# Optimization experiments

Hardware: AMD Instinct MI355X
Metric: run time of the kernel (lower is better)

## Reference

```python
import jax, jax.numpy as jnp
import numpy as np

VAR0, VAR1 = 0.1, 0.2
POS_TH, NEG_TH = 0.5, 0.5
NEG_POS_RATIO = 10

def point_form(c):
    # center-size (cx,cy,w,h) -> corners (x1,y1,x2,y2)
    return jnp.concatenate([c[..., :2] - c[..., 2:] / 2, c[..., :2] + c[..., 2:] / 2], axis=-1)

def iou(a, b):
    # corner-form boxes, broadcastable [..., 4]
    lt = jnp.maximum(a[..., :2], b[..., :2])
    rb = jnp.minimum(a[..., 2:], b[..., 2:])
    wh = jnp.clip(rb - lt, 0.0)
    inter = wh[..., 0] * wh[..., 1]
    area_a = (a[..., 2] - a[..., 0]) * (a[..., 3] - a[..., 1])
    area_b = (b[..., 2] - b[..., 0]) * (b[..., 3] - b[..., 1])
    return inter / (area_a + area_b - inter)

def encode(matched, priors):
    # matched: corner-form gt boxes; priors: center-size anchors
    g_cxcy = ((matched[..., :2] + matched[..., 2:]) * 0.5 - priors[..., :2]) / (VAR0 * priors[..., 2:])
    g_wh = jnp.log((matched[..., 2:] - matched[..., :2]) / priors[..., 2:]) / VAR1
    return jnp.concatenate([g_cxcy, g_wh], axis=-1)

def smooth_l1(d):
    ad = jnp.abs(d)
    return jnp.where(ad < 1.0, 0.5 * ad * ad, ad - 0.5)

def setup_inputs() -> dict:
    key = jax.random.key(0)
    ks = jax.random.split(key, 8)
    B, O, A = 8, 32, 16384
    cxy = jax.random.uniform(ks[0], (A, 2), minval=0.1, maxval=0.9)
    wh = jax.random.uniform(ks[1], (A, 2), minval=0.05, maxval=0.3)
    anchors = jnp.concatenate([cxy, wh], axis=-1)  # [A,4] center-size
    # ground-truth boxes jittered around random anchors so matching finds positives
    idx = jax.random.randint(ks[2], (B, O), 0, A)
    base = point_form(anchors)[idx]  # [B,O,4] corner form
    boxes = base + jax.random.uniform(ks[3], (B, O, 4), minval=-0.01, maxval=0.01)
    counts = jax.random.randint(ks[4], (B,), 4, O)  # valid objects per image
    pad = jnp.arange(O)[None, :] >= counts[:, None]
    cls = jax.random.randint(ks[5], (B, O), 0, 2)
    true_classes = jnp.where(pad, -1, cls).astype(jnp.int32)
    true_boxes = jnp.where(pad[..., None], -1.0, boxes)
    pred_boxes = 0.5 * jax.random.normal(ks[6], (B, A, 4))
    pred_classes = jax.random.normal(ks[7], (B, A, 2))
    return dict(pred_boxes=pred_boxes, pred_classes=pred_classes,
                true_boxes=true_boxes, true_classes=true_classes, anchors=anchors)

def detection_loss(pred_boxes, pred_classes, true_boxes, true_classes, anchors):
    dtype = pred_boxes.dtype
    pad = true_classes < 0  # [B,O]
    # --- anchor matching (IoU between corner-form anchors and gt boxes) ---
    overlap = iou(point_form(anchors)[None, None, :, :], true_boxes[:, :, None, :])  # [B,O,A]
    overlap = jnp.where(pad[..., None], -1.0, overlap)
    best = overlap.max(axis=1, keepdims=True)  # best gt per anchor
    positive = (jnp.abs(best - overlap) < 1e-6) & (overlap > POS_TH)  # [B,O,A]
    negative = overlap.max(axis=1) < NEG_TH  # [B,A]
    n_pos = positive.sum()
    denom = jnp.maximum(n_pos, 1).astype(dtype)
    # --- box loss: SmoothL1(sum) on encoded positives only ---
    dummy = jnp.array([0.3, 0.3, 0.5, 0.5], dtype)  # valid dummy box for padded slots (masked out)
    tb = jnp.where(pad[..., None], dummy, true_boxes)
    enc = encode(tb[:, :, None, :], anchors[None, None, :, :])  # [B,O,A,4]
    d = jnp.where(positive[..., None], pred_boxes[:, None, :, :] - enc, 0.0)
    box_loss = 1.0 * smooth_l1(d).sum() / denom
    # --- class loss: positives + hard-negative mining, weighted CE mean ---
    logp = jax.nn.log_softmax(pred_classes, axis=-1)  # [B,A,2]
    cls = jnp.clip(true_classes, 0, 1)
    ce_pos = -jnp.where((cls == 1)[:, :, None], logp[:, None, :, 1], logp[:, None, :, 0])  # [B,O,A]
    w = jnp.where(cls == 1, 4.0, 1.0)[:, :, None]
    sum_pos = jnp.sum(positive * w * ce_pos)
    wsum_pos = jnp.sum(positive * w)
    # negatives: target class 0 (weight 1); mining rank == CE value
    neg_ce = jnp.where(negative, -logp[..., 0], -jnp.inf).reshape(-1)  # [B*A]
    sorted_desc = jnp.sort(neg_ce)[::-1]
    n_neg = negative.sum()
    k = jnp.minimum(NEG_POS_RATIO * n_pos, n_neg)
    take = jnp.arange(sorted_desc.shape[0]) < k
    sum_neg = jnp.sum(jnp.where(take, sorted_desc, 0.0))
    cls_loss = 10.0 * (sum_pos + sum_neg) / jnp.maximum(wsum_pos + k.astype(dtype), 1e-6) / denom
    total = box_loss + cls_loss
    return box_loss, cls_loss, total

def reference(pred_boxes, pred_classes, true_boxes, true_classes, anchors):
    return detection_loss(pred_boxes, pred_classes, true_boxes, true_classes, anchors)
```

## Files before the change

kernel.cpp:

```cpp
#include <hip/hip_runtime.h>
#include <math.h>

#define NOBJ  32
#define NANCH 16384
#define NTOT  131072
#define MBLK  256
#define NREP  16

#define OFF_SLOTS 64
#define OFF_HC    2112
#define HWORDS    (NREP * 8192)

__device__ __forceinline__ float smooth_l1f(float d) {
    float ad = fabsf(d);
    return ad < 1.0f ? 0.5f * ad * ad : ad - 0.5f;
}

__global__ __launch_bounds__(256) void dl_zero(unsigned int* __restrict__ ws)
{
    int i = blockIdx.x * 256 + threadIdx.x;
    reinterpret_cast<uint4*>(ws + OFF_HC)[i] = make_uint4(0u, 0u, 0u, 0u);
}

__global__ __launch_bounds__(512) void dl_main(
    const float* __restrict__ pred_boxes,
    const float* __restrict__ pred_classes,
    const float* __restrict__ true_boxes,
    const int*   __restrict__ true_classes,
    const float* __restrict__ anchors,
    unsigned int* __restrict__ ws)
{
    __shared__ float    s_tb[NOBJ * 4];
    __shared__ int      s_tc[NOBJ];
    __shared__ unsigned lcnt[4096];
    __shared__ float    lsum[4096];
    __shared__ int      s_wi[8][2];
    __shared__ float    s_wf[8][3];

    const int t = threadIdx.x;
    const int idx = blockIdx.x * 512 + t;
    const int b = idx >> 14;
    const int a = idx & (NANCH - 1);
    if (t < NOBJ * 4) s_tb[t] = true_boxes[b * NOBJ * 4 + t];
    if (t < NOBJ)     s_tc[t] = true_classes[b * NOBJ + t];
    for (int i = t; i < 4096; i += 512) { lcnt[i] = 0u; lsum[i] = 0.f; }
    __syncthreads();

    float4 anc = reinterpret_cast<const float4*>(anchors)[a];
    float ax1 = anc.x - anc.z * 0.5f;
    float ay1 = anc.y - anc.w * 0.5f;
    float ax2 = anc.x + anc.z * 0.5f;
    float ay2 = anc.y + anc.w * 0.5f;
    float area_a = (ax2 - ax1) * (ay2 - ay1);

    float ov[NOBJ];
    float best = -3.402823466e38f;
#pragma unroll
    for (int o = 0; o < NOBJ; ++o) {
        float v;
        if (s_tc[o] < 0) {
            v = -1.0f;
        } else {
            float bx1 = s_tb[o * 4 + 0], by1 = s_tb[o * 4 + 1];
            float bx2 = s_tb[o * 4 + 2], by2 = s_tb[o * 4 + 3];
            float ltx = fmaxf(ax1, bx1), lty = fmaxf(ay1, by1);
            float rbx = fminf(ax2, bx2), rby = fminf(ay2, by2);
            float w = fmaxf(rbx - ltx, 0.0f), h = fmaxf(rby - lty, 0.0f);
            float inter = w * h;
            float area_b = (bx2 - bx1) * (by2 - by1);
            v = inter / (area_a + area_b - inter);
        }
        ov[o] = v;
        best = fmaxf(best, v);
    }

    float2 pc = reinterpret_cast<const float2*>(pred_classes)[idx];
    float mx = fmaxf(pc.x, pc.y);
    float lse = mx + logf(expf(pc.x - mx) + expf(pc.y - mx));
    float l0 = pc.x - lse;
    float l1 = pc.y - lse;

    int isneg = 0;
    if (best < 0.5f) {
        float nce = -l0;
        unsigned bk = (__float_as_uint(nce) >> 19) & 0xFFFu;
        atomicAdd(&lcnt[bk], 1u);
        atomicAdd(&lsum[bk], nce);
        isneg = 1;
    }

    float4 pb = reinterpret_cast<const float4*>(pred_boxes)[idx];
    int npos = 0; float boxs = 0.f, poss = 0.f, wsum = 0.f;
#pragma unroll
    for (int o = 0; o < NOBJ; ++o) {
        float v = ov[o];
        if (fabsf(best - v) < 1e-6f && v > 0.5f) {
            ++npos;
            float bx1 = s_tb[o * 4 + 0], by1 = s_tb[o * 4 + 1];
            float bx2 = s_tb[o * 4 + 2], by2 = s_tb[o * 4 + 3];
            float gcx = ((bx1 + bx2) * 0.5f - anc.x) / (0.1f * anc.z);
            float gcy = ((by1 + by2) * 0.5f - anc.y) / (0.1f * anc.w);
            float gw  = logf((bx2 - bx1) / anc.z) / 0.2f;
            float gh  = logf((by2 - by1) / anc.w) / 0.2f;
            boxs += smooth_l1f(pb.x - gcx) + smooth_l1f(pb.y - gcy)
                  + smooth_l1f(pb.z - gw)  + smooth_l1f(pb.w - gh);
            int c = s_tc[o];
            float w = (c == 1) ? 4.0f : 1.0f;
            poss += w * ((c == 1) ? -l1 : -l0);
            wsum += w;
        }
    }

    int ip = npos, ng = isneg;
    float fb = boxs, fp = poss, fw = wsum;
#pragma unroll
    for (int o = 32; o; o >>= 1) {
        ip += __shfl_down(ip, o); ng += __shfl_down(ng, o);
        fb += __shfl_down(fb, o); fp += __shfl_down(fp, o); fw += __shfl_down(fw, o);
    }
    const int wave = t >> 6, lane = t & 63;
    if (lane == 0) {
        s_wi[wave][0] = ip; s_wi[wave][1] = ng;
        s_wf[wave][0] = fb; s_wf[wave][1] = fp; s_wf[wave][2] = fw;
    }
    __syncthreads();
    if (t == 0) {
        int tp = 0, tn = 0; float t2 = 0.f, t3 = 0.f, t4 = 0.f;
        for (int w = 0; w < 8; ++w) {
            tp += s_wi[w][0]; tn += s_wi[w][1];
            t2 += s_wf[w][0]; t3 += s_wf[w][1]; t4 += s_wf[w][2];
        }
        unsigned* sl = ws + OFF_SLOTS + blockIdx.x * 8;
        sl[0] = (unsigned)tp; sl[1] = (unsigned)tn;
        sl[2] = __float_as_uint(t2); sl[3] = __float_as_uint(t3); sl[4] = __float_as_uint(t4);
    }
    unsigned* gc = ws + OFF_HC + (blockIdx.x & (NREP - 1)) * 8192;
    float*    gs = reinterpret_cast<float*>(gc + 4096);
    for (int i = t; i < 4096; i += 512) {
        unsigned c = lcnt[i];
        if (c) { atomicAdd(gc + i, c); atomicAdd(gs + i, lsum[i]); }
    }
}

__global__ __launch_bounds__(1024) void dl_tail(const unsigned int* __restrict__ ws,
                                                float* __restrict__ out)
{
    __shared__ int   s_wi[16][2];
    __shared__ float s_wf[16][3];
    __shared__ int   wti[16];
    __shared__ float wtf[16];
    __shared__ int   sh_k;
    __shared__ float sh_fp, sh_fw, sh_box, sh_denom;

    const int t = threadIdx.x, wave = t >> 6, lane = t & 63;

    int np = 0, nn = 0; float fb = 0.f, fp = 0.f, fw = 0.f;
    if (t < MBLK) {
        const unsigned* sl = ws + OFF_SLOTS + t * 8;
        np = (int)sl[0]; nn = (int)sl[1];
        fb = __uint_as_float(sl[2]); fp = __uint_as_float(sl[3]); fw = __uint_as_float(sl[4]);
    }
#pragma unroll
    for (int o = 32; o; o >>= 1) {
        np += __shfl_down(np, o); nn += __shfl_down(nn, o);
        fb += __shfl_down(fb, o); fp += __shfl_down(fp, o); fw += __shfl_down(fw, o);
    }
    if (lane == 0 && wave < 4) {
        s_wi[wave][0] = np; s_wi[wave][1] = nn;
        s_wf[wave][0] = fb; s_wf[wave][1] = fp; s_wf[wave][2] = fw;
    }
    __syncthreads();
    if (t == 0) {
        int tp = 0, tn = 0; float t2 = 0.f, t3 = 0.f, t4 = 0.f;
        for (int w = 0; w < 4; ++w) {
            tp += s_wi[w][0]; tn += s_wi[w][1];
            t2 += s_wf[w][0]; t3 += s_wf[w][1]; t4 += s_wf[w][2];
        }
        long long k10 = 10LL * (long long)tp;
        int k = (int)((k10 < (long long)tn) ? k10 : (long long)tn);
        sh_k = k;
        sh_fp = t3; sh_fw = t4;
        sh_denom = (float)(tp > 1 ? tp : 1);
        sh_box = t2 / sh_denom;
    }
    __syncthreads();
    const int k = sh_k;
    if (k == 0) {
        if (t == 0) {
            float cls = 10.0f * sh_fp / fmaxf(sh_fw, 1e-6f) / sh_denom;
            out[0] = sh_box; out[1] = cls; out[2] = sh_box + cls;
        }
        return;
    }

    uint4  c4 = make_uint4(0u, 0u, 0u, 0u);
    float4 s4 = make_float4(0.f, 0.f, 0.f, 0.f);
#pragma unroll
    for (int r = 0; r < NREP; ++r) {
        uint4  u = *reinterpret_cast<const uint4*>(ws + OFF_HC + r * 8192 + t * 4);
        float4 s = *reinterpret_cast<const float4*>(ws + OFF_HC + r * 8192 + 4096 + t * 4);
        c4.x += u.x; c4.y += u.y; c4.z += u.z; c4.w += u.w;
        s4.x += s.x; s4.y += s.y; s4.z += s.z; s4.w += s.w;
    }
    unsigned cbk[4] = { c4.x, c4.y, c4.z, c4.w };
    float    sbk[4] = { s4.x, s4.y, s4.z, s4.w };
    int   cc = (int)(cbk[0] + cbk[1] + cbk[2] + cbk[3]);
    float ss = sbk[0] + sbk[1] + sbk[2] + sbk[3];

    int v = cc; float f = ss;
#pragma unroll
    for (int o = 1; o < 64; o <<= 1) {
        int   u2 = __shfl_down(v, o);
        float g2 = __shfl_down(f, o);
        if (lane + o < 64) { v += u2; f += g2; }
    }
    if (lane == 0) { wti[wave] = v; wtf[wave] = f; }
    __syncthreads();
    int S = v; float FS = f;
    for (int w = wave + 1; w < 16; ++w) { S += wti[w]; FS += wtf[w]; }

    if (S >= k && S - cc < k) {
        int   cum  = S - cc;
        float facc = FS - ss;
        float sfx = 0.f;
        for (int bq = 3; bq >= 0; --bq) {
            int cb = (int)cbk[bq];
            if (cum + cb >= k) {
                int r1 = k - cum;
                float sneg = facc + sfx + (float)r1 * (sbk[bq] / (float)cb);
                float cls = 10.0f * (sh_fp + sneg)
                          / fmaxf(sh_fw + (float)k, 1e-6f) / sh_denom;
                out[0] = sh_box; out[1] = cls; out[2] = sh_box + cls;
                break;
            }
            cum += cb; sfx += sbk[bq];
        }
    }
}

extern "C" void kernel_launch(void* const* d_in, const int* in_sizes, int n_in,
                              void* d_out, int out_size, void* d_ws, size_t ws_size,
                              hipStream_t stream)
{
    const float* pred_boxes   = (const float*)d_in[0];
    const float* pred_classes = (const float*)d_in[1];
    const float* true_boxes   = (const float*)d_in[2];
    const int*   true_classes = (const int*)d_in[3];
    const float* anchors      = (const float*)d_in[4];
    unsigned int* ws = (unsigned int*)d_ws;

    dl_zero<<<128, 256, 0, stream>>>(ws);
    dl_main<<<MBLK, 512, 0, stream>>>(pred_boxes, pred_classes, true_boxes,
                                      true_classes, anchors, ws);
    dl_tail<<<1, 1024, 0, stream>>>(ws, (float*)d_out);
}
```

Baseline: 28.75 us.

## Shrink negative-CE histogram to clamped 2048-bucket range with per-wave LDS replicas

The histogram of negative cross-entropy values now covers an offset, clamped window of 2048 buckets instead of 4096. Shared-memory atomics are split into two replicas by wave parity to reduce contention. There are half as many global replicas, so zeroing, merging and the tail scan touch less data. Clamping out-of-range values into the edge buckets relies on the CE values falling in the covered exponent range, and the tail still interpolates within buckets.

```diff
diff --git a/kernel.cpp b/kernel.cpp
--- a/kernel.cpp
+++ b/kernel.cpp
@@ -5,11 +5,13 @@
 #define NANCH 16384
 #define NTOT  131072
 #define MBLK  256
-#define NREP  16
+#define NREP  8
+#define NBUK  2048
+#define BOFF  1792
 
 #define OFF_SLOTS 64
 #define OFF_HC    2112
-#define HWORDS    (NREP * 8192)
+#define HWORDS    (NREP * NBUK * 2)
 
 __device__ __forceinline__ float smooth_l1f(float d) {
     float ad = fabsf(d);
@@ -32,8 +34,8 @@
 {
     __shared__ float    s_tb[NOBJ * 4];
     __shared__ int      s_tc[NOBJ];
-    __shared__ unsigned lcnt[4096];
-    __shared__ float    lsum[4096];
+    __shared__ unsigned lcnt[2][NBUK];
+    __shared__ float    lsum[2][NBUK];
     __shared__ int      s_wi[8][2];
     __shared__ float    s_wf[8][3];
 
@@ -43,7 +45,7 @@
     const int a = idx & (NANCH - 1);
     if (t < NOBJ * 4) s_tb[t] = true_boxes[b * NOBJ * 4 + t];
     if (t < NOBJ)     s_tc[t] = true_classes[b * NOBJ + t];
-    for (int i = t; i < 4096; i += 512) { lcnt[i] = 0u; lsum[i] = 0.f; }
+    for (int i = t; i < 2 * NBUK; i += 512) { (&lcnt[0][0])[i] = 0u; (&lsum[0][0])[i] = 0.f; }
     __syncthreads();
 
     float4 anc = reinterpret_cast<const float4*>(anchors)[a];
@@ -80,12 +82,14 @@
     float l0 = pc.x - lse;
     float l1 = pc.y - lse;
 
+    const int wave = t >> 6, lane = t & 63, rep = wave & 1;
     int isneg = 0;
     if (best < 0.5f) {
         float nce = -l0;
-        unsigned bk = (__float_as_uint(nce) >> 19) & 0xFFFu;
-        atomicAdd(&lcnt[bk], 1u);
-        atomicAdd(&lsum[bk], nce);
+        int bk = (int)(__float_as_uint(nce) >> 19) - BOFF;
+        bk = bk < 0 ? 0 : (bk > NBUK - 1 ? NBUK - 1 : bk);
+        atomicAdd(&lcnt[rep][bk], 1u);
+        atomicAdd(&lsum[rep][bk], nce);
         isneg = 1;
     }
 
@@ -118,7 +122,6 @@
         ip += __shfl_down(ip, o); ng += __shfl_down(ng, o);
         fb += __shfl_down(fb, o); fp += __shfl_down(fp, o); fw += __shfl_down(fw, o);
     }
-    const int wave = t >> 6, lane = t & 63;
     if (lane == 0) {
         s_wi[wave][0] = ip; s_wi[wave][1] = ng;
         s_wf[wave][0] = fb; s_wf[wave][1] = fp; s_wf[wave][2] = fw;
@@ -134,11 +137,11 @@
         sl[0] = (unsigned)tp; sl[1] = (unsigned)tn;
         sl[2] = __float_as_uint(t2); sl[3] = __float_as_uint(t3); sl[4] = __float_as_uint(t4);
     }
-    unsigned* gc = ws + OFF_HC + (blockIdx.x & (NREP - 1)) * 8192;
-    float*    gs = reinterpret_cast<float*>(gc + 4096);
-    for (int i = t; i < 4096; i += 512) {
-        unsigned c = lcnt[i];
-        if (c) { atomicAdd(gc + i, c); atomicAdd(gs + i, lsum[i]); }
+    unsigned* gc = ws + OFF_HC + (blockIdx.x & (NREP - 1)) * (NBUK * 2);
+    float*    gs = reinterpret_cast<float*>(gc + NBUK);
+    for (int i = t; i < NBUK; i += 512) {
+        unsigned c = lcnt[0][i] + lcnt[1][i];
+        if (c) { atomicAdd(gc + i, c); atomicAdd(gs + i, lsum[0][i] + lsum[1][i]); }
     }
 }
 
@@ -193,19 +196,17 @@
         return;
     }
 
-    uint4  c4 = make_uint4(0u, 0u, 0u, 0u);
-    float4 s4 = make_float4(0.f, 0.f, 0.f, 0.f);
+    unsigned cbk[2] = {0u, 0u};
+    float    sbk[2] = {0.f, 0.f};
 #pragma unroll
     for (int r = 0; r < NREP; ++r) {
-        uint4  u = *reinterpret_cast<const uint4*>(ws + OFF_HC + r * 8192 + t * 4);
-        float4 s = *reinterpret_cast<const float4*>(ws + OFF_HC + r * 8192 + 4096 + t * 4);
-        c4.x += u.x; c4.y += u.y; c4.z += u.z; c4.w += u.w;
-        s4.x += s.x; s4.y += s.y; s4.z += s.z; s4.w += s.w;
-    }
-    unsigned cbk[4] = { c4.x, c4.y, c4.z, c4.w };
-    float    sbk[4] = { s4.x, s4.y, s4.z, s4.w };
-    int   cc = (int)(cbk[0] + cbk[1] + cbk[2] + cbk[3]);
-    float ss = sbk[0] + sbk[1] + sbk[2] + sbk[3];
+        uint2  u = *reinterpret_cast<const uint2*>(ws + OFF_HC + r * (NBUK * 2) + t * 2);
+        float2 s = *reinterpret_cast<const float2*>(ws + OFF_HC + r * (NBUK * 2) + NBUK + t * 2);
+        cbk[0] += u.x; cbk[1] += u.y;
+        sbk[0] += s.x; sbk[1] += s.y;
+    }
+    int   cc = (int)(cbk[0] + cbk[1]);
+    float ss = sbk[0] + sbk[1];
 
     int v = cc; float f = ss;
 #pragma unroll
@@ -223,7 +224,7 @@
         int   cum  = S - cc;
         float facc = FS - ss;
         float sfx = 0.f;
-        for (int bq = 3; bq >= 0; --bq) {
+        for (int bq = 1; bq >= 0; --bq) {
             int cb = (int)cbk[bq];
             if (cum + cb >= k) {
                 int r1 = k - cum;
@@ -249,7 +250,7 @@
     const float* anchors      = (const float*)d_in[4];
     unsigned int* ws = (unsigned int*)d_ws;
 
-    dl_zero<<<128, 256, 0, stream>>>(ws);
+    dl_zero<<<32, 256, 0, stream>>>(ws);
     dl_main<<<MBLK, 512, 0, stream>>>(pred_boxes, pred_classes, true_boxes,
                                       true_classes, anchors, ws);
     dl_tail<<<1, 1024, 0, stream>>>(ws, (float*)d_out);
```

Measured after the change: 26.21 us, median of 2. 1.1x faster.
